# Kernel tuning notes

Measured on AMD Instinct MI355X. Metric: run time of the kernel, lower is better.

Reference implementation:

```python
import jax, jax.numpy as jnp
import numpy as np

T_SIZE = 64
S_SIZE = 256
NUM_HEADS = 12
DEPTH = 12
DIM = 768
MLP_DIM = 3072
EPS = 1e-5
BATCH = 32
N_TOK = 2 * T_SIZE + S_SIZE  # 384


def setup_inputs() -> dict:
    key = jax.random.key(0)
    ks = jax.random.split(key, 6)
    s = 0.02
    return {
        "x": jax.random.normal(ks[0], (BATCH, N_TOK, DIM), jnp.float32),
        "qkv_w": jax.random.normal(ks[1], (DEPTH, DIM, 3 * DIM), jnp.float32) * s,
        "qkv_b": jnp.zeros((DEPTH, 3 * DIM), jnp.float32),
        "proj_w": jax.random.normal(ks[2], (DEPTH, DIM, DIM), jnp.float32) * s,
        "proj_b": jnp.zeros((DEPTH, DIM), jnp.float32),
        "ln1_g": jnp.ones((DEPTH, DIM), jnp.float32),
        "ln1_b": jnp.zeros((DEPTH, DIM), jnp.float32),
        "ln2_g": jnp.ones((DEPTH, DIM), jnp.float32),
        "ln2_b": jnp.zeros((DEPTH, DIM), jnp.float32),
        "fc1_w": jax.random.normal(ks[3], (DEPTH, DIM, MLP_DIM), jnp.float32) * s,
        "fc1_b": jnp.zeros((DEPTH, MLP_DIM), jnp.float32),
        "fc2_w": jax.random.normal(ks[4], (DEPTH, MLP_DIM, DIM), jnp.float32) * s,
        "fc2_b": jnp.zeros((DEPTH, DIM), jnp.float32),
    }


def _layernorm(x, g, b):
    m = jnp.mean(x, axis=-1, keepdims=True)
    v = jnp.mean((x - m) ** 2, axis=-1, keepdims=True)
    return (x - m) * jax.lax.rsqrt(v + EPS) * g + b


def _attention(x, wqkv, bqkv, wp, bp):
    B, N, C = x.shape
    hd = C // NUM_HEADS
    scale = hd ** -0.5
    # [B,N,3C] -> [3,B,H,N,hd]
    qkv = (x @ wqkv + bqkv).reshape(B, N, 3, NUM_HEADS, hd).transpose(2, 0, 3, 1, 4)
    q, k, v = qkv[0], qkv[1], qkv[2]
    q_t = q[:, :, :T_SIZE]
    q_it = q[:, :, T_SIZE:2 * T_SIZE]
    q_s = q[:, :, 2 * T_SIZE:]
    k_it = k[:, :, T_SIZE:2 * T_SIZE]
    v_it = v[:, :, T_SIZE:2 * T_SIZE]
    # mix attention: (t, s) queries over ALL keys
    q_ts = jnp.concatenate([q_t, q_s], axis=2)  # [B,H,t+s,hd]
    mix = jax.nn.softmax(jnp.einsum('bhqd,bhkd->bhqk', q_ts, k) * scale, axis=-1)
    ts = jnp.einsum('bhqk,bhkd->bhqd', mix, v).transpose(0, 2, 1, 3).reshape(B, T_SIZE + S_SIZE, C)
    # inherent attention: it queries over it keys only
    inh = jax.nn.softmax(jnp.einsum('bhqd,bhkd->bhqk', q_it, k_it) * scale, axis=-1)
    it = jnp.einsum('bhqk,bhkd->bhqd', inh, v_it).transpose(0, 2, 1, 3).reshape(B, T_SIZE, C)
    out = jnp.concatenate([ts[:, :T_SIZE], it, ts[:, T_SIZE:]], axis=1)
    return out @ wp + bp


def reference(x, qkv_w, qkv_b, proj_w, proj_b, ln1_g, ln1_b, ln2_g, ln2_b,
              fc1_w, fc1_b, fc2_w, fc2_b):
    for l in range(DEPTH):
        x = x + _attention(_layernorm(x, ln1_g[l], ln1_b[l]),
                           qkv_w[l], qkv_b[l], proj_w[l], proj_b[l])
        h = _layernorm(x, ln2_g[l], ln2_b[l])
        h = jax.nn.gelu(h @ fc1_w[l] + fc1_b[l], approximate=False)
        x = x + (h @ fc2_w[l] + fc2_b[l])
    return x
```

## Files before the change

kernel.cpp:

```cpp
#include <hip/hip_runtime.h>
#include <cstdint>

typedef unsigned short u16;
typedef __attribute__((ext_vector_type(8))) short bf16x8;
typedef __attribute__((ext_vector_type(4))) float f32x4;

#define B_SZ 32
#define NTOK 384
#define DIM 768
#define NH 12
#define HD 64
#define MLP 3072
#define MROWS (B_SZ * NTOK)

__device__ __forceinline__ float b2f(u16 h) { return __uint_as_float(((unsigned)h) << 16); }
__device__ __forceinline__ u16 f2b(float f) {
    unsigned u = __float_as_uint(f);
    unsigned r = u + 0x7fffu + ((u >> 16) & 1u);
    return (u16)(r >> 16);
}

__device__ __forceinline__ void load_lds16(const void* g, void* l) {
    __builtin_amdgcn_global_load_lds(
        (const __attribute__((address_space(1))) unsigned*)g,
        (__attribute__((address_space(3))) unsigned*)l, 16, 0, 0);
}

__device__ __forceinline__ float gelu_fast(float v) {
    float u2 = -1.5957691216f * v * (1.0f + 0.044715f * v * v);
    return v * __builtin_amdgcn_rcpf(1.0f + __expf(u2));
}

__global__ void detect_kernel(const u16* __restrict__ x, int* __restrict__ flagp) {
    __shared__ int cnt;
    if (threadIdx.x == 0) cnt = 0;
    __syncthreads();
    int bad = 0;
    for (int i = threadIdx.x; i < 4096; i += 256) {
        int e = (x[i] >> 7) & 0xFF;
        if (e >= 0xC0) bad++;
    }
    atomicAdd(&cnt, bad);
    __syncthreads();
    if (threadIdx.x == 0) *flagp = (cnt > 4) ? 1 : 0;
}

__global__ void conv_any(const void* __restrict__ src, u16* __restrict__ dst, int n,
                         const int* __restrict__ flagp) {
    int i = blockIdx.x * 256 + threadIdx.x;
    if (i >= n) return;
    dst[i] = (*flagp) ? f2b(((const float*)src)[i]) : ((const u16*)src)[i];
}

__global__ void load_x(const void* __restrict__ src, float* __restrict__ dst, int n,
                       const int* __restrict__ flagp) {
    int i = blockIdx.x * 256 + threadIdx.x;
    if (i >= n) return;
    dst[i] = (*flagp) ? ((const float*)src)[i] : b2f(((const u16*)src)[i]);
}

__global__ void store_out(const float* __restrict__ src, void* __restrict__ dst, int n,
                          const int* __restrict__ flagp) {
    int i = blockIdx.x * 256 + threadIdx.x;
    if (i >= n) return;
    if (*flagp) ((float*)dst)[i] = src[i];
    else ((u16*)dst)[i] = f2b(src[i]);
}

__global__ __launch_bounds__(256) void transpose_k(const void* __restrict__ in, size_t ioff,
                                                   u16* __restrict__ outp, int K, int N,
                                                   const int* __restrict__ flagp) {
    __shared__ u16 t[32][33];
    const int flag = *flagp;
    const int n0 = blockIdx.x << 5, k0 = blockIdx.y << 5;
    const int tx = threadIdx.x, ty = threadIdx.y;
#pragma unroll
    for (int i = 0; i < 4; i++) {
        size_t idx = ioff + (size_t)(k0 + ty + i * 8) * N + n0 + tx;
        t[ty + i * 8][tx] = flag ? f2b(((const float*)in)[idx]) : ((const u16*)in)[idx];
    }
    __syncthreads();
#pragma unroll
    for (int i = 0; i < 4; i++)
        outp[(size_t)(n0 + ty + i * 8) * K + k0 + tx] = t[tx][ty + i * 8];
}

template <int MODE, int TM>
__global__ __launch_bounds__(256) void gemm_bt(const u16* __restrict__ A,
                                               const u16* __restrict__ Bt,
                                               const u16* __restrict__ bias,
                                               u16* __restrict__ outb,
                                               float* __restrict__ outf,
                                               int N, int K) {
    constexpr int MI = (TM == 128) ? 4 : 2;
    constexpr int AT = (TM == 128) ? 4 : 2;
    __shared__ u16 lA[TM * 64];
    __shared__ u16 lB[128 * 64];
    const int tid = threadIdx.x;
    const int wave = tid >> 6, lane = tid & 63;
    const int quad = lane >> 4, l16 = lane & 15;

    const int gx = gridDim.x;
    const int nwg = gx * gridDim.y;
    const int orig = blockIdx.y * gx + blockIdx.x;
    const int xcd = orig & 7, loc = orig >> 3;
    const int qq = nwg >> 3, rr = nwg & 7;
    const int wgid = (xcd < rr ? xcd * (qq + 1) : rr * (qq + 1) + (xcd - rr) * qq) + loc;
    const int bx = wgid % gx, by = wgid / gx;

    const int m0 = by * TM, n0 = bx << 7;
    const int wm = (wave & 1) * (TM / 2), wn = (wave >> 1) << 6;
    const int lr = lane >> 3;
    const int swz = ((lane & 7) ^ lr) << 3;

    f32x4 acc[MI][4] = {};

    const u16* gA = A + (size_t)(m0 + wave * (8 * AT) + lr) * K + swz;
    const u16* gB = Bt + (size_t)(n0 + wave * 32 + lr) * K + swz;

    for (int kt = 0; kt < K; kt += 64) {
        __syncthreads();
#pragma unroll
        for (int t = 0; t < AT; t++)
            load_lds16(gA + kt + (size_t)t * 8 * K, &lA[(wave * AT + t) * 512 + lane * 8]);
#pragma unroll
        for (int t = 0; t < 4; t++)
            load_lds16(gB + kt + (size_t)t * 8 * K, &lB[(wave * 4 + t) * 512 + lane * 8]);
        __syncthreads();
        const int xs = l16 & 7;
#pragma unroll
        for (int kk = 0; kk < 2; kk++) {
            bf16x8 af[MI], bfr[4];
            const int ksel = ((kk << 2) + quad);
#pragma unroll
            for (int i = 0; i < MI; i++)
                af[i] = *(const bf16x8*)&lA[(wm + i * 16 + l16) * 64 + ((ksel ^ xs) << 3)];
#pragma unroll
            for (int j = 0; j < 4; j++)
                bfr[j] = *(const bf16x8*)&lB[(wn + j * 16 + l16) * 64 + ((ksel ^ xs) << 3)];
#pragma unroll
            for (int i = 0; i < MI; i++)
#pragma unroll
                for (int j = 0; j < 4; j++)
                    acc[i][j] = __builtin_amdgcn_mfma_f32_16x16x32_bf16(af[i], bfr[j], acc[i][j], 0, 0, 0);
        }
    }

#pragma unroll
    for (int j = 0; j < 4; j++) {
        const int n = n0 + wn + j * 16 + l16;
        const float bv = b2f(bias[n]);
#pragma unroll
        for (int i = 0; i < MI; i++) {
            const int mrow = m0 + wm + i * 16 + quad * 4;
#pragma unroll
            for (int r = 0; r < 4; r++) {
                float v = acc[i][j][r] + bv;
                size_t idx = (size_t)(mrow + r) * N + n;
                if (MODE == 0) {
                    outb[idx] = f2b(v);
                } else if (MODE == 1) {
                    outb[idx] = f2b(gelu_fast(v));
                } else {
                    outf[idx] += v;
                }
            }
        }
    }
}

__global__ __launch_bounds__(256) void ln_kernel(const float* __restrict__ x,
                                                 const u16* __restrict__ g,
                                                 const u16* __restrict__ bta,
                                                 u16* __restrict__ y) {
    const int wave = threadIdx.x >> 6, lane = threadIdx.x & 63;
    const int row = (blockIdx.x << 2) + wave;
    const float4* xr = (const float4*)(x + (size_t)row * DIM);
    float4 v[3];
    float s = 0.f, sq = 0.f;
#pragma unroll
    for (int i = 0; i < 3; i++) {
        v[i] = xr[i * 64 + lane];
        s += v[i].x + v[i].y + v[i].z + v[i].w;
        sq += v[i].x * v[i].x + v[i].y * v[i].y + v[i].z * v[i].z + v[i].w * v[i].w;
    }
#pragma unroll
    for (int off = 32; off >= 1; off >>= 1) {
        s += __shfl_xor(s, off, 64);
        sq += __shfl_xor(sq, off, 64);
    }
    const float mean = s * (1.f / DIM);
    const float var = sq * (1.f / DIM) - mean * mean;
    const float rs = rsqrtf(var + 1e-5f);
    u16* yr = y + (size_t)row * DIM;
#pragma unroll
    for (int i = 0; i < 3; i++) {
        ushort4 gg = ((const ushort4*)g)[i * 64 + lane];
        ushort4 bb = ((const ushort4*)bta)[i * 64 + lane];
        ushort4 o;
        o.x = f2b((v[i].x - mean) * rs * b2f(gg.x) + b2f(bb.x));
        o.y = f2b((v[i].y - mean) * rs * b2f(gg.y) + b2f(bb.y));
        o.z = f2b((v[i].z - mean) * rs * b2f(gg.z) + b2f(bb.z));
        o.w = f2b((v[i].w - mean) * rs * b2f(gg.w) + b2f(bb.w));
        ((ushort4*)yr)[i * 64 + lane] = o;
    }
}

template <int NJ, int JLO>
__global__ __launch_bounds__(256) void attn_kernel(const u16* __restrict__ qkv,
                                                   u16* __restrict__ out) {
    constexpr int K0 = JLO * 16;
    constexpr int NKEY = NJ * 16;
    constexpr int VSTR = NKEY + 8;
    __shared__ u16 vT[64 * VSTR];
    __shared__ u16 pbuf[4][16 * 76];
    const int tid = threadIdx.x, wave = tid >> 6, lane = tid & 63;
    const int quad = lane >> 4, l16 = lane & 15;

    int qt, h, b;
    if (NJ == 24) {
        const int id = blockIdx.x + 5 * (blockIdx.y + 12 * blockIdx.z);
        const int xcd = id & 7, slot = id >> 3;
        const int ppx = (int)(gridDim.x * gridDim.y * gridDim.z) >> 3;
        const int s5 = slot / 5;
        const int pair = xcd * (ppx / 5) + s5;
        const int qi = slot - 5 * s5;
        qt = qi + (qi >= 1 ? 1 : 0);
        h = pair % 12;
        b = pair / 12;
    } else {
        qt = 1; h = blockIdx.y; b = blockIdx.z;
    }
    const u16* base = qkv + (size_t)b * NTOK * (3 * DIM);

    for (int it = tid; it < NKEY * 8; it += 256) {
        const int kk = it >> 3, dseg = it & 7;
        const u16* gp = base + (size_t)(K0 + kk) * (3 * DIM) + 2 * DIM + h * HD + dseg * 8;
        ushort4 u0 = ((const ushort4*)gp)[0];
        ushort4 u1 = ((const ushort4*)gp)[1];
        u16 vals[8] = {u0.x, u0.y, u0.z, u0.w, u1.x, u1.y, u1.z, u1.w};
#pragma unroll
        for (int t = 0; t < 8; t++) {
            const int i = (t + kk + dseg) & 7;
            vT[(dseg * 8 + i) * VSTR + kk] = vals[i];
        }
    }

    bf16x8 qf[2];
    const int qrow = qt * 64 + wave * 16 + l16;
#pragma unroll
    for (int s = 0; s < 2; s++)
        qf[s] = *(const bf16x8*)(base + (size_t)qrow * (3 * DIM) + h * HD + s * 32 + quad * 8);

    __syncthreads();

    f32x4 sacc[NJ];
#pragma unroll
    for (int j = 0; j < NJ; j++) {
        const int key = (JLO + j) * 16 + l16;
        const u16* kb = base + (size_t)key * (3 * DIM) + DIM + h * HD;
        bf16x8 k0 = *(const bf16x8*)(kb + quad * 8);
        bf16x8 k1 = *(const bf16x8*)(kb + 32 + quad * 8);
        f32x4 z = {0.f, 0.f, 0.f, 0.f};
        z = __builtin_amdgcn_mfma_f32_16x16x32_bf16(qf[0], k0, z, 0, 0, 0);
        sacc[j] = __builtin_amdgcn_mfma_f32_16x16x32_bf16(qf[1], k1, z, 0, 0, 0);
    }

    float mx[4] = {-1e30f, -1e30f, -1e30f, -1e30f};
#pragma unroll
    for (int j = 0; j < NJ; j++)
#pragma unroll
        for (int r = 0; r < 4; r++) mx[r] = fmaxf(mx[r], sacc[j][r]);
#pragma unroll
    for (int off = 1; off < 16; off <<= 1)
#pragma unroll
        for (int r = 0; r < 4; r++) mx[r] = fmaxf(mx[r], __shfl_xor(mx[r], off, 64));

    float sm[4] = {0.f, 0.f, 0.f, 0.f};
#pragma unroll
    for (int j = 0; j < NJ; j++)
#pragma unroll
        for (int r = 0; r < 4; r++) {
            float e = __expf((sacc[j][r] - mx[r]) * 0.125f);
            sacc[j][r] = e;
            sm[r] += e;
        }
#pragma unroll
    for (int off = 1; off < 16; off <<= 1)
#pragma unroll
        for (int r = 0; r < 4; r++) sm[r] += __shfl_xor(sm[r], off, 64);
    float inv[4];
#pragma unroll
    for (int r = 0; r < 4; r++) inv[r] = 1.f / sm[r];

    f32x4 oacc[4] = {};
    u16* pb = &pbuf[wave][0];
#pragma unroll
    for (int c = 0; c < NJ / 4; c++) {
#pragma unroll
        for (int jj = 0; jj < 4; jj++) {
#pragma unroll
            for (int r = 0; r < 4; r++)
                pb[(quad * 4 + r) * 76 + jj * 16 + l16] = f2b(sacc[c * 4 + jj][r] * inv[r]);
        }
#pragma unroll
        for (int s = 0; s < 2; s++) {
            bf16x8 pf = *(const bf16x8*)&pb[l16 * 76 + s * 32 + quad * 8];
            const int kc = c * 64 + s * 32 + quad * 8;
#pragma unroll
            for (int jd = 0; jd < 4; jd++) {
                bf16x8 vf = *(const bf16x8*)&vT[(jd * 16 + l16) * VSTR + kc];
                oacc[jd] = __builtin_amdgcn_mfma_f32_16x16x32_bf16(pf, vf, oacc[jd], 0, 0, 0);
            }
        }
    }

    const int q = qt * 64 + wave * 16 + quad * 4;
    u16* orow = out + (size_t)(b * NTOK + q) * DIM + h * HD;
#pragma unroll
    for (int jd = 0; jd < 4; jd++)
#pragma unroll
        for (int r = 0; r < 4; r++)
            orow[(size_t)r * DIM + jd * 16 + l16] = f2b(oacc[jd][r]);
}

extern "C" void kernel_launch(void* const* d_in, const int* in_sizes, int n_in,
                              void* d_out, int out_size, void* d_ws, size_t ws_size,
                              hipStream_t stream) {
    const void* x_in   = d_in[0];
    const void* qkv_w  = d_in[1];
    const void* qkv_b  = d_in[2];
    const void* proj_w = d_in[3];
    const void* proj_b = d_in[4];
    const void* ln1_g  = d_in[5];
    const void* ln1_b  = d_in[6];
    const void* ln2_g  = d_in[7];
    const void* ln2_b  = d_in[8];
    const void* fc1_w  = d_in[9];
    const void* fc1_b  = d_in[10];
    const void* fc2_w  = d_in[11];
    const void* fc2_b  = d_in[12];

    constexpr size_t SZ_X32 = (size_t)MROWS * DIM * 4;
    constexpr size_t SZ_ABUF = (size_t)MROWS * DIM * 2;
    constexpr size_t SZ_BIG = (size_t)MROWS * MLP * 2;
    constexpr size_t SZ_WT = (size_t)(2304 * 768 + 768 * 768 + 3072 * 768 + 768 * 3072) * 2;
    constexpr size_t SZ_PAR = 262144;
    const size_t fixed = SZ_X32 + SZ_ABUF + SZ_WT + SZ_PAR + 256;

    int nc;
    if (fixed + SZ_BIG <= ws_size) nc = 1;
    else if (fixed + SZ_BIG / 2 <= ws_size) nc = 2;
    else nc = 4;
    const size_t bigsz = SZ_BIG / nc;

    char* ws = (char*)d_ws;
    float* x32 = (float*)ws;
    u16* abuf = (u16*)(ws + SZ_X32);
    u16* big = (u16*)(ws + SZ_X32 + SZ_ABUF);
    u16* wqt = (u16*)(ws + SZ_X32 + SZ_ABUF + bigsz);
    u16* wpt = wqt + 2304 * 768;
    u16* w1t = wpt + 768 * 768;
    u16* w2t = w1t + 3072 * 768;
    u16* par = w2t + 768 * 3072;
    int* flagp = (int*)((char*)(par) + SZ_PAR);

    u16* p_qkvb = par;
    u16* p_projb = p_qkvb + 12 * 2304;
    u16* p_ln1g = p_projb + 12 * 768;
    u16* p_ln1b = p_ln1g + 12 * 768;
    u16* p_ln2g = p_ln1b + 12 * 768;
    u16* p_ln2b = p_ln2g + 12 * 768;
    u16* p_fc1b = p_ln2b + 12 * 768;
    u16* p_fc2b = p_fc1b + 12 * 3072;

    const int NEL = MROWS * DIM;
    detect_kernel<<<1, 256, 0, stream>>>((const u16*)x_in, flagp);
    load_x<<<(NEL + 255) / 256, 256, 0, stream>>>(x_in, x32, NEL, flagp);
    conv_any<<<(12 * 2304 + 255) / 256, 256, 0, stream>>>(qkv_b, p_qkvb, 12 * 2304, flagp);
    conv_any<<<(12 * 768 + 255) / 256, 256, 0, stream>>>(proj_b, p_projb, 12 * 768, flagp);
    conv_any<<<(12 * 768 + 255) / 256, 256, 0, stream>>>(ln1_g, p_ln1g, 12 * 768, flagp);
    conv_any<<<(12 * 768 + 255) / 256, 256, 0, stream>>>(ln1_b, p_ln1b, 12 * 768, flagp);
    conv_any<<<(12 * 768 + 255) / 256, 256, 0, stream>>>(ln2_g, p_ln2g, 12 * 768, flagp);
    conv_any<<<(12 * 768 + 255) / 256, 256, 0, stream>>>(ln2_b, p_ln2b, 12 * 768, flagp);
    conv_any<<<(12 * 3072 + 255) / 256, 256, 0, stream>>>(fc1_b, p_fc1b, 12 * 3072, flagp);
    conv_any<<<(12 * 768 + 255) / 256, 256, 0, stream>>>(fc2_b, p_fc2b, 12 * 768, flagp);

    const int CR = MROWS / nc;
    const int CB = B_SZ / nc;

    for (int l = 0; l < 12; l++) {
        transpose_k<<<dim3(2304 / 32, 768 / 32), dim3(32, 8), 0, stream>>>(
            qkv_w, (size_t)l * DIM * 2304, wqt, DIM, 2304, flagp);
        transpose_k<<<dim3(768 / 32, 768 / 32), dim3(32, 8), 0, stream>>>(
            proj_w, (size_t)l * DIM * DIM, wpt, DIM, DIM, flagp);
        transpose_k<<<dim3(3072 / 32, 768 / 32), dim3(32, 8), 0, stream>>>(
            fc1_w, (size_t)l * DIM * MLP, w1t, DIM, MLP, flagp);
        transpose_k<<<dim3(768 / 32, 3072 / 32), dim3(32, 8), 0, stream>>>(
            fc2_w, (size_t)l * MLP * DIM, w2t, MLP, DIM, flagp);

        for (int c = 0; c < nc; c++) {
            const size_t r0 = (size_t)c * CR;
            ln_kernel<<<CR / 4, 256, 0, stream>>>(x32 + r0 * DIM, p_ln1g + l * DIM,
                                                  p_ln1b + l * DIM, abuf + r0 * DIM);
            gemm_bt<0, 128><<<dim3(2304 / 128, CR / 128), 256, 0, stream>>>(
                abuf + r0 * DIM, wqt, p_qkvb + l * 2304, big, nullptr, 2304, DIM);
            attn_kernel<24, 0><<<dim3(5, NH, CB), 256, 0, stream>>>(big, abuf + r0 * DIM);
            attn_kernel<4, 4><<<dim3(1, NH, CB), 256, 0, stream>>>(big, abuf + r0 * DIM);
            gemm_bt<2, 64><<<dim3(DIM / 128, CR / 64), 256, 0, stream>>>(
                abuf + r0 * DIM, wpt, p_projb + l * DIM, nullptr, x32 + r0 * DIM, DIM, DIM);
        }
        for (int c = 0; c < nc; c++) {
            const size_t r0 = (size_t)c * CR;
            ln_kernel<<<CR / 4, 256, 0, stream>>>(x32 + r0 * DIM, p_ln2g + l * DIM,
                                                  p_ln2b + l * DIM, abuf + r0 * DIM);
            gemm_bt<1, 128><<<dim3(MLP / 128, CR / 128), 256, 0, stream>>>(
                abuf + r0 * DIM, w1t, p_fc1b + l * MLP, big, nullptr, MLP, DIM);
            gemm_bt<2, 64><<<dim3(DIM / 128, CR / 64), 256, 0, stream>>>(
                big, w2t, p_fc2b + l * DIM, nullptr, x32 + r0 * DIM, DIM, MLP);
        }
    }
    store_out<<<(NEL + 255) / 256, 256, 0, stream>>>(x32, d_out, NEL, flagp);
}
```

Measured before the change: 5.187 ms.

## Stage V in chunked rounds with XOR-swizzled LDS transpose in attention

```diff
diff --git a/kernel.cpp b/kernel.cpp
--- a/kernel.cpp
+++ b/kernel.cpp
@@ -211,7 +211,10 @@
                                                    u16* __restrict__ out) {
     constexpr int K0 = JLO * 16;
     constexpr int NKEY = NJ * 16;
-    constexpr int VSTR = NKEY + 8;
+    constexpr int KCH = (NJ == 24) ? 192 : 64;
+    constexpr int NROUNDS = NKEY / KCH;
+    constexpr int CPR = KCH / 64;
+    constexpr int VSTR = KCH + 8;
     __shared__ u16 vT[64 * VSTR];
     __shared__ u16 pbuf[4][16 * 76];
     const int tid = threadIdx.x, wave = tid >> 6, lane = tid & 63;
@@ -233,18 +236,21 @@
     }
     const u16* base = qkv + (size_t)b * NTOK * (3 * DIM);
 
-    for (int it = tid; it < NKEY * 8; it += 256) {
-        const int kk = it >> 3, dseg = it & 7;
-        const u16* gp = base + (size_t)(K0 + kk) * (3 * DIM) + 2 * DIM + h * HD + dseg * 8;
-        ushort4 u0 = ((const ushort4*)gp)[0];
-        ushort4 u1 = ((const ushort4*)gp)[1];
-        u16 vals[8] = {u0.x, u0.y, u0.z, u0.w, u1.x, u1.y, u1.z, u1.w};
-#pragma unroll
-        for (int t = 0; t < 8; t++) {
-            const int i = (t + kk + dseg) & 7;
-            vT[(dseg * 8 + i) * VSTR + kk] = vals[i];
-        }
-    }
+    auto stage_v = [&](int kbase) {
+        for (int it = tid; it < KCH * 8; it += 256) {
+            const int kklo = it & 7, dseg = (it >> 3) & 7, kkhi = it >> 6;
+            const int kk = (kkhi << 3) | kklo;
+            const u16* gp = base + (size_t)(kbase + kk) * (3 * DIM) + 2 * DIM + h * HD + dseg * 8;
+            const uint4 w = *(const uint4*)gp;
+            u16* wp = &vT[(dseg * 8) * VSTR + (kk ^ (dseg << 3))];
+            wp[0 * VSTR] = (u16)w.x; wp[1 * VSTR] = (u16)(w.x >> 16);
+            wp[2 * VSTR] = (u16)w.y; wp[3 * VSTR] = (u16)(w.y >> 16);
+            wp[4 * VSTR] = (u16)w.z; wp[5 * VSTR] = (u16)(w.z >> 16);
+            wp[6 * VSTR] = (u16)w.w; wp[7 * VSTR] = (u16)(w.w >> 16);
+        }
+    };
+
+    stage_v(K0);
 
     bf16x8 qf[2];
     const int qrow = qt * 64 + wave * 16 + l16;
@@ -296,21 +302,31 @@
     f32x4 oacc[4] = {};
     u16* pb = &pbuf[wave][0];
 #pragma unroll
-    for (int c = 0; c < NJ / 4; c++) {
-#pragma unroll
-        for (int jj = 0; jj < 4; jj++) {
-#pragma unroll
-            for (int r = 0; r < 4; r++)
-                pb[(quad * 4 + r) * 76 + jj * 16 + l16] = f2b(sacc[c * 4 + jj][r] * inv[r]);
-        }
-#pragma unroll
-        for (int s = 0; s < 2; s++) {
-            bf16x8 pf = *(const bf16x8*)&pb[l16 * 76 + s * 32 + quad * 8];
-            const int kc = c * 64 + s * 32 + quad * 8;
-#pragma unroll
-            for (int jd = 0; jd < 4; jd++) {
-                bf16x8 vf = *(const bf16x8*)&vT[(jd * 16 + l16) * VSTR + kc];
-                oacc[jd] = __builtin_amdgcn_mfma_f32_16x16x32_bf16(pf, vf, oacc[jd], 0, 0, 0);
+    for (int rd = 0; rd < NROUNDS; rd++) {
+        if (rd > 0) {
+            __syncthreads();
+            stage_v(K0 + rd * KCH);
+            __syncthreads();
+        }
+#pragma unroll
+        for (int cl = 0; cl < CPR; cl++) {
+            const int c = rd * CPR + cl;
+#pragma unroll
+            for (int jj = 0; jj < 4; jj++) {
+#pragma unroll
+                for (int r = 0; r < 4; r++)
+                    pb[(quad * 4 + r) * 76 + jj * 16 + l16] = f2b(sacc[c * 4 + jj][r] * inv[r]);
+            }
+#pragma unroll
+            for (int s = 0; s < 2; s++) {
+                bf16x8 pf = *(const bf16x8*)&pb[l16 * 76 + s * 32 + quad * 8];
+                const int lc = cl * 64 + s * 32 + quad * 8;
+#pragma unroll
+                for (int jd = 0; jd < 4; jd++) {
+                    const int key8 = (jd * 2 + (l16 >> 3)) & 7;
+                    bf16x8 vf = *(const bf16x8*)&vT[(jd * 16 + l16) * VSTR + (lc ^ (key8 << 3))];
+                    oacc[jd] = __builtin_amdgcn_mfma_f32_16x16x32_bf16(pf, vf, oacc[jd], 0, 0, 0);
+                }
             }
         }
     }
```

After: 5.211 ms. About the same (+0.5%).
